# Kernel tuning notes

Hardware: AMD Instinct MI355X
Metric: run time of the kernel (lower is better)

## Reference

```python
import jax, jax.numpy as jnp
import numpy as np

N_NODES = 10000
N_EDGES = 320000
IN_DIM = 256
HIDDEN = 256
OUT_DIM = 128


def setup_inputs() -> dict:
    key = jax.random.key(0)
    k1, k2, k3, k4, k5, k6 = jax.random.split(key, 6)
    features = jax.random.normal(k1, (N_NODES, IN_DIM), dtype=jnp.float32)
    edge_src = jax.random.randint(k2, (N_EDGES,), 0, N_NODES, dtype=jnp.int64)
    edge_dst = jax.random.randint(k3, (N_EDGES,), 0, N_NODES, dtype=jnp.int64)
    edge_val = jax.random.uniform(k4, (N_EDGES,), dtype=jnp.float32)
    # Xavier-uniform weights as in nn.init.xavier_uniform_
    lim0 = float(np.sqrt(6.0 / (IN_DIM + HIDDEN)))
    lim1 = float(np.sqrt(6.0 / (HIDDEN + OUT_DIM)))
    W0 = jax.random.uniform(k5, (IN_DIM, HIDDEN), dtype=jnp.float32, minval=-lim0, maxval=lim0)
    W1 = jax.random.uniform(k6, (HIDDEN, OUT_DIM), dtype=jnp.float32, minval=-lim1, maxval=lim1)
    return {"features": features, "edge_src": edge_src, "edge_dst": edge_dst,
            "edge_val": edge_val, "W0": W0, "W1": W1}


def reference(features, edge_src, edge_dst, edge_val, W0, W1):
    # Sum over partition SpMMs in `broadcast` == full-graph SpMM: Z = A @ H
    n = features.shape[0]

    def spmm(h):
        msgs = edge_val[:, None] * h[edge_src]          # [E, d] gather + scale
        return jax.ops.segment_sum(msgs, edge_dst, num_segments=n)  # [N, d] scatter-add

    h = jax.nn.relu(spmm(features) @ W0)  # layer 0: SpMM -> GEMM -> ReLU
    out = spmm(h) @ W1                    # layer 1 (last): SpMM -> GEMM, no ReLU
    return out
```

## Files before the change

### kernel.cpp

```cpp
#include <hip/hip_runtime.h>

#define N_NODES 10000
#define IN_DIM 256
#define HIDDEN 256
#define OUT_DIM 128

typedef __attribute__((ext_vector_type(8))) short bf16x8;
typedef __attribute__((ext_vector_type(4))) float f32x4;
typedef __attribute__((ext_vector_type(4))) unsigned short u16x4;

__device__ __forceinline__ unsigned short f2bf(float x) {
  union { float f; unsigned u; } c; c.f = x;
  unsigned r = (c.u + 0x7FFFu + ((c.u >> 16) & 1u)) >> 16;
  return (unsigned short)r;
}
__device__ __forceinline__ float bf2f(unsigned short u) {
  union { unsigned u; float f; } c; c.u = ((unsigned)u) << 16;
  return c.f;
}

__global__ __launch_bounds__(256)
void hist_convW(const int* __restrict__ dst, int* __restrict__ cnt,
                const float* __restrict__ W0, const float* __restrict__ W1,
                unsigned short* __restrict__ W0t, unsigned short* __restrict__ W1t,
                int nE) {
  int gid = blockIdx.x * 256 + threadIdx.x;
  if (gid < nE) atomicAdd(&cnt[dst[gid]], 1);
  if (gid < IN_DIM * HIDDEN) {
    int k = gid & 255, n = gid >> 8;
    W0t[n * 256 + k] = f2bf(W0[k * 256 + n]);
  } else if (gid < IN_DIM * HIDDEN + HIDDEN * OUT_DIM) {
    int i = gid - IN_DIM * HIDDEN;
    int k = i & 255, n = i >> 8;
    W1t[n * 256 + k] = f2bf(W1[k * 128 + n]);
  }
}

__global__ __launch_bounds__(1024)
void scan_kernel(const int* __restrict__ cnt, int* __restrict__ rowptr,
                 int* __restrict__ rowcur) {
  const int t = threadIdx.x;
  const int lane = t & 63, wv = t >> 6;
  constexpr int PER = 10;
  const int base = t * PER;
  int c[PER];
  int sum = 0;
#pragma unroll
  for (int i = 0; i < PER; ++i) {
    int idx = base + i;
    c[i] = (idx < N_NODES) ? cnt[idx] : 0;
    sum += c[i];
  }
  int x = sum;
  for (int off = 1; off < 64; off <<= 1) {
    int y = __shfl_up(x, off);
    if (lane >= off) x += y;
  }
  __shared__ int wsum[16], wpre[16];
  if (lane == 63) wsum[wv] = x;
  __syncthreads();
  if (t == 0) {
    int run = 0;
#pragma unroll
    for (int i = 0; i < 16; ++i) { wpre[i] = run; run += wsum[i]; }
  }
  __syncthreads();
  int run = wpre[wv] + x - sum;
#pragma unroll
  for (int i = 0; i < PER; ++i) {
    int idx = base + i;
    if (idx < N_NODES) {
      rowptr[idx] = run;
      rowcur[idx] = run;
      run += c[i];
    }
  }
  if (t == 1023) rowptr[N_NODES] = run;
}

__global__ __launch_bounds__(256)
void bucket_kernel(const int* __restrict__ src, const int* __restrict__ dst,
                   const float* __restrict__ val, int* __restrict__ rowcur,
                   int2* __restrict__ edges, int nE) {
  int i = blockIdx.x * 256 + threadIdx.x;
  if (i < nE) {
    int d = dst[i];
    int p = atomicAdd(&rowcur[d], 1);
    edges[p] = make_int2(src[i], __float_as_int(val[i]));
  }
}

__global__ __launch_bounds__(256)
void gemm_mfma(const float* __restrict__ F, const unsigned short* __restrict__ Bt,
               unsigned short* __restrict__ C) {
  const int w = threadIdx.x >> 6;
  const int l = threadIdx.x & 63;
  const int r0 = blockIdx.y * 64 + w * 16;
  const int c0 = blockIdx.x * 64;
  const int arow = r0 + (l & 15);
  const int kof = (l >> 4) * 8;
  const bool rv = arow < N_NODES;
  const float* Ap = F + (size_t)arow * 256 + kof;
  f32x4 acc[4] = {};
#pragma unroll
  for (int k0 = 0; k0 < 256; k0 += 32) {
    bf16x8 af = {};
    if (rv) {
      float4 fa = *reinterpret_cast<const float4*>(Ap + k0);
      float4 fb = *reinterpret_cast<const float4*>(Ap + k0 + 4);
      af[0] = (short)f2bf(fa.x); af[1] = (short)f2bf(fa.y);
      af[2] = (short)f2bf(fa.z); af[3] = (short)f2bf(fa.w);
      af[4] = (short)f2bf(fb.x); af[5] = (short)f2bf(fb.y);
      af[6] = (short)f2bf(fb.z); af[7] = (short)f2bf(fb.w);
    }
#pragma unroll
    for (int j = 0; j < 4; ++j) {
      bf16x8 bfr = *reinterpret_cast<const bf16x8*>(
          Bt + (size_t)(c0 + j * 16 + (l & 15)) * 256 + k0 + kof);
      acc[j] = __builtin_amdgcn_mfma_f32_16x16x32_bf16(af, bfr, acc[j], 0, 0, 0);
    }
  }
  const int orow0 = r0 + ((l >> 4) << 2);
#pragma unroll
  for (int j = 0; j < 4; ++j) {
    const int col = c0 + j * 16 + (l & 15);
#pragma unroll
    for (int r = 0; r < 4; ++r) {
      int orow = orow0 + r;
      if (orow < N_NODES) C[(size_t)orow * HIDDEN + col] = f2bf(acc[j][r]);
    }
  }
}

__global__ __launch_bounds__(512)
void fused_spmm_gemm(const unsigned short* __restrict__ T0b,
                     const int2* __restrict__ edges,
                     const int* __restrict__ rp,
                     const unsigned short* __restrict__ W1t,
                     unsigned short* __restrict__ T1b) {
  __shared__ unsigned short Zs[16 * 256];
  const int wv = threadIdx.x >> 6;
  const int l  = threadIdx.x & 63;
  const int nb = blockIdx.x * 16;
  const unsigned short* Xl = T0b + l * 4;
#pragma unroll
  for (int i = 0; i < 2; ++i) {
    const int r = wv * 2 + i;
    const int node = nb + r;
    const int r0 = rp[node], r1 = rp[node + 1];
    float acc[4] = {};
    for (int base = r0; base < r1; base += 64) {
      int m = r1 - base; if (m > 64) m = 64;
      int2 me = make_int2(0, 0);
      if (base + l < r1) me = edges[base + l];
      int j = 0;
      for (; j + 4 <= m; j += 4) {
        int s0 = __shfl(me.x, j + 0), s1 = __shfl(me.x, j + 1);
        int s2 = __shfl(me.x, j + 2), s3 = __shfl(me.x, j + 3);
        float v0 = __int_as_float(__shfl(me.y, j + 0));
        float v1 = __int_as_float(__shfl(me.y, j + 1));
        float v2 = __int_as_float(__shfl(me.y, j + 2));
        float v3 = __int_as_float(__shfl(me.y, j + 3));
        u16x4 a = *reinterpret_cast<const u16x4*>(Xl + (size_t)s0 * 256);
        u16x4 b = *reinterpret_cast<const u16x4*>(Xl + (size_t)s1 * 256);
        u16x4 c = *reinterpret_cast<const u16x4*>(Xl + (size_t)s2 * 256);
        u16x4 d = *reinterpret_cast<const u16x4*>(Xl + (size_t)s3 * 256);
#pragma unroll
        for (int q = 0; q < 4; ++q) acc[q] = fmaf(v0, bf2f(a[q]), acc[q]);
#pragma unroll
        for (int q = 0; q < 4; ++q) acc[q] = fmaf(v1, bf2f(b[q]), acc[q]);
#pragma unroll
        for (int q = 0; q < 4; ++q) acc[q] = fmaf(v2, bf2f(c[q]), acc[q]);
#pragma unroll
        for (int q = 0; q < 4; ++q) acc[q] = fmaf(v3, bf2f(d[q]), acc[q]);
      }
      for (; j < m; ++j) {
        int s0 = __shfl(me.x, j);
        float v0 = __int_as_float(__shfl(me.y, j));
        u16x4 a = *reinterpret_cast<const u16x4*>(Xl + (size_t)s0 * 256);
#pragma unroll
        for (int q = 0; q < 4; ++q) acc[q] = fmaf(v0, bf2f(a[q]), acc[q]);
      }
    }
    u16x4 o;
#pragma unroll
    for (int q = 0; q < 4; ++q) o[q] = f2bf(fmaxf(acc[q], 0.f));
    int off = (r * 512 + l * 8) ^ ((r & 7) << 4);
    *reinterpret_cast<u16x4*>(reinterpret_cast<char*>(Zs) + off) = o;
  }
  __syncthreads();
  const int row = l & 15;
  const int kof = (l >> 4) * 8;
  const int cb = wv * 16;
  f32x4 acc2 = {};
#pragma unroll
  for (int k0 = 0; k0 < 256; k0 += 32) {
    int aoff = (row * 512 + (k0 + kof) * 2) ^ ((row & 7) << 4);
    bf16x8 af = *reinterpret_cast<const bf16x8*>(reinterpret_cast<const char*>(Zs) + aoff);
    bf16x8 bfr = *reinterpret_cast<const bf16x8*>(
        W1t + (size_t)(cb + row) * 256 + k0 + kof);
    acc2 = __builtin_amdgcn_mfma_f32_16x16x32_bf16(af, bfr, acc2, 0, 0, 0);
  }
  const int orow0 = (l >> 4) * 4;
  const int col = cb + row;
#pragma unroll
  for (int rr = 0; rr < 4; ++rr)
    T1b[(size_t)(nb + orow0 + rr) * OUT_DIM + col] = f2bf(acc2[rr]);
}

__global__ __launch_bounds__(256)
void spmm_out(const unsigned short* __restrict__ T1b,
              const int2* __restrict__ edges,
              const int* __restrict__ rp,
              float* __restrict__ out) {
  const int wv = threadIdx.x >> 6;
  const int lane = threadIdx.x & 63;
  const int half = lane >> 5;
  const int hl = lane & 31;
  const int node = blockIdx.x * 8 + wv * 2 + half;
  const int r0 = rp[node], r1 = rp[node + 1];
  float acc[4] = {};
  const unsigned short* Xl = T1b + hl * 4;
  for (int base = r0; base < r1; base += 32) {
    int m = r1 - base; if (m > 32) m = 32;
    int2 me = make_int2(0, 0);
    if (base + hl < r1) me = edges[base + hl];
    int j = 0;
    for (; j + 4 <= m; j += 4) {
      int s0 = __shfl(me.x, j + 0, 32), s1 = __shfl(me.x, j + 1, 32);
      int s2 = __shfl(me.x, j + 2, 32), s3 = __shfl(me.x, j + 3, 32);
      float v0 = __int_as_float(__shfl(me.y, j + 0, 32));
      float v1 = __int_as_float(__shfl(me.y, j + 1, 32));
      float v2 = __int_as_float(__shfl(me.y, j + 2, 32));
      float v3 = __int_as_float(__shfl(me.y, j + 3, 32));
      u16x4 a = *reinterpret_cast<const u16x4*>(Xl + (size_t)s0 * 128);
      u16x4 b = *reinterpret_cast<const u16x4*>(Xl + (size_t)s1 * 128);
      u16x4 c = *reinterpret_cast<const u16x4*>(Xl + (size_t)s2 * 128);
      u16x4 d = *reinterpret_cast<const u16x4*>(Xl + (size_t)s3 * 128);
#pragma unroll
      for (int q = 0; q < 4; ++q) acc[q] = fmaf(v0, bf2f(a[q]), acc[q]);
#pragma unroll
      for (int q = 0; q < 4; ++q) acc[q] = fmaf(v1, bf2f(b[q]), acc[q]);
#pragma unroll
      for (int q = 0; q < 4; ++q) acc[q] = fmaf(v2, bf2f(c[q]), acc[q]);
#pragma unroll
      for (int q = 0; q < 4; ++q) acc[q] = fmaf(v3, bf2f(d[q]), acc[q]);
    }
    for (; j < m; ++j) {
      int s0 = __shfl(me.x, j, 32);
      float v0 = __int_as_float(__shfl(me.y, j, 32));
      u16x4 a = *reinterpret_cast<const u16x4*>(Xl + (size_t)s0 * 128);
#pragma unroll
      for (int q = 0; q < 4; ++q) acc[q] = fmaf(v0, bf2f(a[q]), acc[q]);
    }
  }
  float4 o; o.x = acc[0]; o.y = acc[1]; o.z = acc[2]; o.w = acc[3];
  *reinterpret_cast<float4*>(out + (size_t)node * OUT_DIM + hl * 4) = o;
}

extern "C" void kernel_launch(void* const* d_in, const int* in_sizes, int n_in,
                              void* d_out, int out_size, void* d_ws, size_t ws_size,
                              hipStream_t stream) {
  const float* features = (const float*)d_in[0];
  const int*   esrc     = (const int*)d_in[1];
  const int*   edst     = (const int*)d_in[2];
  const float* evalv    = (const float*)d_in[3];
  const float* W0       = (const float*)d_in[4];
  const float* W1       = (const float*)d_in[5];
  const int nE = in_sizes[1];
  float* out = (float*)d_out;

  unsigned short* W0t = (unsigned short*)d_ws;
  unsigned short* W1t = W0t + (size_t)IN_DIM * HIDDEN;
  unsigned short* T0b = W1t + (size_t)OUT_DIM * HIDDEN;
  unsigned short* T1b = T0b + (size_t)N_NODES * HIDDEN;
  int2* edges  = (int2*)(T1b + (size_t)N_NODES * OUT_DIM);
  int* cnt     = (int*)(edges + nE);
  int* rowptr  = cnt + N_NODES;
  int* rowcur  = rowptr + N_NODES + 1;

  const int ebk = (nE + 255) / 256;

  hipMemsetAsync(cnt, 0, N_NODES * sizeof(int), stream);
  hist_convW<<<ebk, 256, 0, stream>>>(edst, cnt, W0, W1, W0t, W1t, nE);
  scan_kernel<<<1, 1024, 0, stream>>>(cnt, rowptr, rowcur);
  bucket_kernel<<<ebk, 256, 0, stream>>>(esrc, edst, evalv, rowcur, edges, nE);

  gemm_mfma<<<dim3(HIDDEN / 64, (N_NODES + 63) / 64), 256, 0, stream>>>(features, W0t, T0b);
  fused_spmm_gemm<<<N_NODES / 16, 512, 0, stream>>>(T0b, edges, rowptr, W1t, T1b);
  spmm_out<<<N_NODES / 8, 256, 0, stream>>>(T1b, edges, rowptr, out);
}
```

Baseline: 173.9 us.

## Merge all stages into one persistent cooperative kernel with grid syncs

Replaces the memset and six separate kernel launches with a single cooperative persistent kernel that walks through each stage and separates them with grid.sync(). The edge histogram now runs at the same time as the first dense GEMM, split across disjoint block groups. The fused SpMM+GEMM stage moves from 512-thread blocks to 256-thread blocks doing more work per wave. The goal is to remove launch gaps and tail idling between short kernels. In exchange it adds grid-wide barrier costs, caps occupancy through the cooperative launch size, and runs the row-pointer scan on a single block while the rest of the grid waits.

```diff
diff --git a/kernel.cpp b/kernel.cpp
--- a/kernel.cpp
+++ b/kernel.cpp
@@ -1,4 +1,7 @@
 #include <hip/hip_runtime.h>
+#include <hip/hip_cooperative_groups.h>
+
+namespace cg = cooperative_groups;
 
 #define N_NODES 10000
 #define IN_DIM 256
@@ -19,152 +22,223 @@
   return c.f;
 }
 
-__global__ __launch_bounds__(256)
-void hist_convW(const int* __restrict__ dst, int* __restrict__ cnt,
-                const float* __restrict__ W0, const float* __restrict__ W1,
-                unsigned short* __restrict__ W0t, unsigned short* __restrict__ W1t,
-                int nE) {
-  int gid = blockIdx.x * 256 + threadIdx.x;
-  if (gid < nE) atomicAdd(&cnt[dst[gid]], 1);
-  if (gid < IN_DIM * HIDDEN) {
-    int k = gid & 255, n = gid >> 8;
-    W0t[n * 256 + k] = f2bf(W0[k * 256 + n]);
-  } else if (gid < IN_DIM * HIDDEN + HIDDEN * OUT_DIM) {
-    int i = gid - IN_DIM * HIDDEN;
+__global__ __launch_bounds__(256, 3)
+void uber(const float* __restrict__ F, const int* __restrict__ esrc,
+          const int* __restrict__ edst, const float* __restrict__ evalv,
+          const float* __restrict__ W0, const float* __restrict__ W1,
+          float* __restrict__ out,
+          unsigned short* W0t, unsigned short* W1t,
+          unsigned short* T0b, unsigned short* T1b,
+          int2* edges, int* cnt, int* rowptr, int* rowcur, int nE) {
+  cg::grid_group grid = cg::this_grid();
+  __shared__ unsigned short Zs[16 * 256];
+  const int bid = blockIdx.x;
+  const int t = threadIdx.x;
+  const int gid0 = bid * 256 + t;
+  const int gstr = gridDim.x * 256;
+  const int wv = t >> 6;
+  const int l = t & 63;
+
+  for (int i = gid0; i < N_NODES; i += gstr) cnt[i] = 0;
+  for (int i = gid0; i < IN_DIM * HIDDEN; i += gstr) {
     int k = i & 255, n = i >> 8;
-    W1t[n * 256 + k] = f2bf(W1[k * 128 + n]);
-  }
-}
-
-__global__ __launch_bounds__(1024)
-void scan_kernel(const int* __restrict__ cnt, int* __restrict__ rowptr,
-                 int* __restrict__ rowcur) {
-  const int t = threadIdx.x;
-  const int lane = t & 63, wv = t >> 6;
-  constexpr int PER = 10;
-  const int base = t * PER;
-  int c[PER];
-  int sum = 0;
-#pragma unroll
-  for (int i = 0; i < PER; ++i) {
-    int idx = base + i;
-    c[i] = (idx < N_NODES) ? cnt[idx] : 0;
-    sum += c[i];
-  }
-  int x = sum;
-  for (int off = 1; off < 64; off <<= 1) {
-    int y = __shfl_up(x, off);
-    if (lane >= off) x += y;
-  }
-  __shared__ int wsum[16], wpre[16];
-  if (lane == 63) wsum[wv] = x;
-  __syncthreads();
-  if (t == 0) {
-    int run = 0;
-#pragma unroll
-    for (int i = 0; i < 16; ++i) { wpre[i] = run; run += wsum[i]; }
-  }
-  __syncthreads();
-  int run = wpre[wv] + x - sum;
-#pragma unroll
-  for (int i = 0; i < PER; ++i) {
-    int idx = base + i;
-    if (idx < N_NODES) {
-      rowptr[idx] = run;
-      rowcur[idx] = run;
-      run += c[i];
-    }
-  }
-  if (t == 1023) rowptr[N_NODES] = run;
-}
-
-__global__ __launch_bounds__(256)
-void bucket_kernel(const int* __restrict__ src, const int* __restrict__ dst,
-                   const float* __restrict__ val, int* __restrict__ rowcur,
-                   int2* __restrict__ edges, int nE) {
-  int i = blockIdx.x * 256 + threadIdx.x;
-  if (i < nE) {
-    int d = dst[i];
+    W0t[i] = f2bf(W0[k * 256 + n]);
+  }
+  for (int i = gid0; i < OUT_DIM * HIDDEN; i += gstr) {
+    int k = i & 255, n = i >> 8;
+    W1t[i] = f2bf(W1[k * 128 + n]);
+  }
+  grid.sync();
+
+  if (bid < 64) {
+    for (int i = gid0; i < nE; i += 64 * 256) atomicAdd(&cnt[edst[i]], 1);
+  } else {
+    for (int tile = bid - 64; tile < 628; tile += gridDim.x - 64) {
+      const int by = tile >> 2, bx = tile & 3;
+      const int r0t = by * 64 + wv * 16;
+      const int c0 = bx * 64;
+      const int arow = r0t + (l & 15);
+      const int kof = (l >> 4) * 8;
+      const bool rv = arow < N_NODES;
+      const float* Ap = F + (size_t)arow * 256 + kof;
+      f32x4 acc[4] = {};
+#pragma unroll
+      for (int k0 = 0; k0 < 256; k0 += 32) {
+        bf16x8 af = {};
+        if (rv) {
+          float4 fa = *reinterpret_cast<const float4*>(Ap + k0);
+          float4 fb = *reinterpret_cast<const float4*>(Ap + k0 + 4);
+          af[0] = (short)f2bf(fa.x); af[1] = (short)f2bf(fa.y);
+          af[2] = (short)f2bf(fa.z); af[3] = (short)f2bf(fa.w);
+          af[4] = (short)f2bf(fb.x); af[5] = (short)f2bf(fb.y);
+          af[6] = (short)f2bf(fb.z); af[7] = (short)f2bf(fb.w);
+        }
+#pragma unroll
+        for (int j = 0; j < 4; ++j) {
+          bf16x8 bfr = *reinterpret_cast<const bf16x8*>(
+              W0t + (size_t)(c0 + j * 16 + (l & 15)) * 256 + k0 + kof);
+          acc[j] = __builtin_amdgcn_mfma_f32_16x16x32_bf16(af, bfr, acc[j], 0, 0, 0);
+        }
+      }
+      const int orow0 = r0t + ((l >> 4) << 2);
+#pragma unroll
+      for (int j = 0; j < 4; ++j) {
+        const int col = c0 + j * 16 + (l & 15);
+#pragma unroll
+        for (int r = 0; r < 4; ++r) {
+          int orow = orow0 + r;
+          if (orow < N_NODES) T0b[(size_t)orow * HIDDEN + col] = f2bf(acc[j][r]);
+        }
+      }
+    }
+  }
+  grid.sync();
+
+  if (bid == 0) {
+    constexpr int PER = (N_NODES + 255) / 256;
+    const int base = t * PER;
+    int c[PER];
+    int sum = 0;
+#pragma unroll
+    for (int i = 0; i < PER; ++i) {
+      int idx = base + i;
+      c[i] = (idx < N_NODES) ? cnt[idx] : 0;
+      sum += c[i];
+    }
+    int x = sum;
+    for (int off = 1; off < 64; off <<= 1) {
+      int y = __shfl_up(x, off);
+      if (l >= off) x += y;
+    }
+    __shared__ int wsum[4], wpre[4];
+    if (l == 63) wsum[wv] = x;
+    __syncthreads();
+    if (t == 0) {
+      int run = 0;
+#pragma unroll
+      for (int i = 0; i < 4; ++i) { wpre[i] = run; run += wsum[i]; }
+    }
+    __syncthreads();
+    int run = wpre[wv] + x - sum;
+#pragma unroll
+    for (int i = 0; i < PER; ++i) {
+      int idx = base + i;
+      if (idx < N_NODES) {
+        rowptr[idx] = run;
+        rowcur[idx] = run;
+        run += c[i];
+      }
+    }
+    if (t == 255) rowptr[N_NODES] = run;
+  }
+  grid.sync();
+
+  for (int i = gid0; i < nE; i += gstr) {
+    int d = edst[i];
     int p = atomicAdd(&rowcur[d], 1);
-    edges[p] = make_int2(src[i], __float_as_int(val[i]));
-  }
-}
-
-__global__ __launch_bounds__(256)
-void gemm_mfma(const float* __restrict__ F, const unsigned short* __restrict__ Bt,
-               unsigned short* __restrict__ C) {
-  const int w = threadIdx.x >> 6;
-  const int l = threadIdx.x & 63;
-  const int r0 = blockIdx.y * 64 + w * 16;
-  const int c0 = blockIdx.x * 64;
-  const int arow = r0 + (l & 15);
-  const int kof = (l >> 4) * 8;
-  const bool rv = arow < N_NODES;
-  const float* Ap = F + (size_t)arow * 256 + kof;
-  f32x4 acc[4] = {};
-#pragma unroll
-  for (int k0 = 0; k0 < 256; k0 += 32) {
-    bf16x8 af = {};
-    if (rv) {
-      float4 fa = *reinterpret_cast<const float4*>(Ap + k0);
-      float4 fb = *reinterpret_cast<const float4*>(Ap + k0 + 4);
-      af[0] = (short)f2bf(fa.x); af[1] = (short)f2bf(fa.y);
-      af[2] = (short)f2bf(fa.z); af[3] = (short)f2bf(fa.w);
-      af[4] = (short)f2bf(fb.x); af[5] = (short)f2bf(fb.y);
-      af[6] = (short)f2bf(fb.z); af[7] = (short)f2bf(fb.w);
-    }
-#pragma unroll
-    for (int j = 0; j < 4; ++j) {
-      bf16x8 bfr = *reinterpret_cast<const bf16x8*>(
-          Bt + (size_t)(c0 + j * 16 + (l & 15)) * 256 + k0 + kof);
-      acc[j] = __builtin_amdgcn_mfma_f32_16x16x32_bf16(af, bfr, acc[j], 0, 0, 0);
-    }
-  }
-  const int orow0 = r0 + ((l >> 4) << 2);
-#pragma unroll
-  for (int j = 0; j < 4; ++j) {
-    const int col = c0 + j * 16 + (l & 15);
-#pragma unroll
-    for (int r = 0; r < 4; ++r) {
-      int orow = orow0 + r;
-      if (orow < N_NODES) C[(size_t)orow * HIDDEN + col] = f2bf(acc[j][r]);
-    }
-  }
-}
-
-__global__ __launch_bounds__(512)
-void fused_spmm_gemm(const unsigned short* __restrict__ T0b,
-                     const int2* __restrict__ edges,
-                     const int* __restrict__ rp,
-                     const unsigned short* __restrict__ W1t,
-                     unsigned short* __restrict__ T1b) {
-  __shared__ unsigned short Zs[16 * 256];
-  const int wv = threadIdx.x >> 6;
-  const int l  = threadIdx.x & 63;
-  const int nb = blockIdx.x * 16;
-  const unsigned short* Xl = T0b + l * 4;
-#pragma unroll
-  for (int i = 0; i < 2; ++i) {
-    const int r = wv * 2 + i;
-    const int node = nb + r;
-    const int r0 = rp[node], r1 = rp[node + 1];
+    edges[p] = make_int2(esrc[i], __float_as_int(evalv[i]));
+  }
+  grid.sync();
+
+  for (int tile = bid; tile < N_NODES / 16; tile += gridDim.x) {
+    const int nb = tile * 16;
+    const unsigned short* Xl = T0b + l * 4;
+#pragma unroll
+    for (int i = 0; i < 4; ++i) {
+      const int r = wv * 4 + i;
+      const int node = nb + r;
+      const int r0 = rowptr[node], r1 = rowptr[node + 1];
+      float acc[4] = {};
+      for (int base = r0; base < r1; base += 64) {
+        int m = r1 - base; if (m > 64) m = 64;
+        int2 me = make_int2(0, 0);
+        if (base + l < r1) me = edges[base + l];
+        int j = 0;
+        for (; j + 4 <= m; j += 4) {
+          int s0 = __shfl(me.x, j + 0), s1 = __shfl(me.x, j + 1);
+          int s2 = __shfl(me.x, j + 2), s3 = __shfl(me.x, j + 3);
+          float v0 = __int_as_float(__shfl(me.y, j + 0));
+          float v1 = __int_as_float(__shfl(me.y, j + 1));
+          float v2 = __int_as_float(__shfl(me.y, j + 2));
+          float v3 = __int_as_float(__shfl(me.y, j + 3));
+          u16x4 a = *reinterpret_cast<const u16x4*>(Xl + (size_t)s0 * 256);
+          u16x4 b = *reinterpret_cast<const u16x4*>(Xl + (size_t)s1 * 256);
+          u16x4 c = *reinterpret_cast<const u16x4*>(Xl + (size_t)s2 * 256);
+          u16x4 d = *reinterpret_cast<const u16x4*>(Xl + (size_t)s3 * 256);
+#pragma unroll
+          for (int q = 0; q < 4; ++q) acc[q] = fmaf(v0, bf2f(a[q]), acc[q]);
+#pragma unroll
+          for (int q = 0; q < 4; ++q) acc[q] = fmaf(v1, bf2f(b[q]), acc[q]);
+#pragma unroll
+          for (int q = 0; q < 4; ++q) acc[q] = fmaf(v2, bf2f(c[q]), acc[q]);
+#pragma unroll
+          for (int q = 0; q < 4; ++q) acc[q] = fmaf(v3, bf2f(d[q]), acc[q]);
+        }
+        for (; j < m; ++j) {
+          int s0 = __shfl(me.x, j);
+          float v0 = __int_as_float(__shfl(me.y, j));
+          u16x4 a = *reinterpret_cast<const u16x4*>(Xl + (size_t)s0 * 256);
+#pragma unroll
+          for (int q = 0; q < 4; ++q) acc[q] = fmaf(v0, bf2f(a[q]), acc[q]);
+        }
+      }
+      u16x4 o;
+#pragma unroll
+      for (int q = 0; q < 4; ++q) o[q] = f2bf(fmaxf(acc[q], 0.f));
+      int off = (r * 512 + l * 8) ^ ((r & 7) << 4);
+      *reinterpret_cast<u16x4*>(reinterpret_cast<char*>(Zs) + off) = o;
+    }
+    __syncthreads();
+    const int row = l & 15;
+    const int kof = (l >> 4) * 8;
+    const int cb = wv * 32;
+    f32x4 acc2[2] = {};
+#pragma unroll
+    for (int k0 = 0; k0 < 256; k0 += 32) {
+      int aoff = (row * 512 + (k0 + kof) * 2) ^ ((row & 7) << 4);
+      bf16x8 af = *reinterpret_cast<const bf16x8*>(reinterpret_cast<const char*>(Zs) + aoff);
+#pragma unroll
+      for (int j = 0; j < 2; ++j) {
+        bf16x8 bfr = *reinterpret_cast<const bf16x8*>(
+            W1t + (size_t)(cb + j * 16 + row) * 256 + k0 + kof);
+        acc2[j] = __builtin_amdgcn_mfma_f32_16x16x32_bf16(af, bfr, acc2[j], 0, 0, 0);
+      }
+    }
+    const int orow0 = (l >> 4) * 4;
+#pragma unroll
+    for (int j = 0; j < 2; ++j) {
+      const int col = cb + j * 16 + row;
+#pragma unroll
+      for (int rr = 0; rr < 4; ++rr)
+        T1b[(size_t)(nb + orow0 + rr) * OUT_DIM + col] = f2bf(acc2[j][rr]);
+    }
+    __syncthreads();
+  }
+  grid.sync();
+
+  for (int tile = bid; tile < N_NODES / 8; tile += gridDim.x) {
+    const int half = l >> 5;
+    const int hl = l & 31;
+    const int node = tile * 8 + wv * 2 + half;
+    const int r0 = rowptr[node], r1 = rowptr[node + 1];
     float acc[4] = {};
-    for (int base = r0; base < r1; base += 64) {
-      int m = r1 - base; if (m > 64) m = 64;
+    const unsigned short* Xl = T1b + hl * 4;
+    for (int base = r0; base < r1; base += 32) {
+      int m = r1 - base; if (m > 32) m = 32;
       int2 me = make_int2(0, 0);
-      if (base + l < r1) me = edges[base + l];
+      if (base + hl < r1) me = edges[base + hl];
       int j = 0;
       for (; j + 4 <= m; j += 4) {
-        int s0 = __shfl(me.x, j + 0), s1 = __shfl(me.x, j + 1);
-        int s2 = __shfl(me.x, j + 2), s3 = __shfl(me.x, j + 3);
-        float v0 = __int_as_float(__shfl(me.y, j + 0));
-        float v1 = __int_as_float(__shfl(me.y, j + 1));
-        float v2 = __int_as_float(__shfl(me.y, j + 2));
-        float v3 = __int_as_float(__shfl(me.y, j + 3));
-        u16x4 a = *reinterpret_cast<const u16x4*>(Xl + (size_t)s0 * 256);
-        u16x4 b = *reinterpret_cast<const u16x4*>(Xl + (size_t)s1 * 256);
-        u16x4 c = *reinterpret_cast<const u16x4*>(Xl + (size_t)s2 * 256);
-        u16x4 d = *reinterpret_cast<const u16x4*>(Xl + (size_t)s3 * 256);
+        int s0 = __shfl(me.x, j + 0, 32), s1 = __shfl(me.x, j + 1, 32);
+        int s2 = __shfl(me.x, j + 2, 32), s3 = __shfl(me.x, j + 3, 32);
+        float v0 = __int_as_float(__shfl(me.y, j + 0, 32));
+        float v1 = __int_as_float(__shfl(me.y, j + 1, 32));
+        float v2 = __int_as_float(__shfl(me.y, j + 2, 32));
+        float v3 = __int_as_float(__shfl(me.y, j + 3, 32));
+        u16x4 a = *reinterpret_cast<const u16x4*>(Xl + (size_t)s0 * 128);
+        u16x4 b = *reinterpret_cast<const u16x4*>(Xl + (size_t)s1 * 128);
+        u16x4 c = *reinterpret_cast<const u16x4*>(Xl + (size_t)s2 * 128);
+        u16x4 d = *reinterpret_cast<const u16x4*>(Xl + (size_t)s3 * 128);
 #pragma unroll
         for (int q = 0; q < 4; ++q) acc[q] = fmaf(v0, bf2f(a[q]), acc[q]);
 #pragma unroll
@@ -175,87 +249,16 @@
         for (int q = 0; q < 4; ++q) acc[q] = fmaf(v3, bf2f(d[q]), acc[q]);
       }
       for (; j < m; ++j) {
-        int s0 = __shfl(me.x, j);
-        float v0 = __int_as_float(__shfl(me.y, j));
-        u16x4 a = *reinterpret_cast<const u16x4*>(Xl + (size_t)s0 * 256);
+        int s0 = __shfl(me.x, j, 32);
+        float v0 = __int_as_float(__shfl(me.y, j, 32));
+        u16x4 a = *reinterpret_cast<const u16x4*>(Xl + (size_t)s0 * 128);
 #pragma unroll
         for (int q = 0; q < 4; ++q) acc[q] = fmaf(v0, bf2f(a[q]), acc[q]);
       }
     }
-    u16x4 o;
-#pragma unroll
-    for (int q = 0; q < 4; ++q) o[q] = f2bf(fmaxf(acc[q], 0.f));
-    int off = (r * 512 + l * 8) ^ ((r & 7) << 4);
-    *reinterpret_cast<u16x4*>(reinterpret_cast<char*>(Zs) + off) = o;
-  }
-  __syncthreads();
-  const int row = l & 15;
-  const int kof = (l >> 4) * 8;
-  const int cb = wv * 16;
-  f32x4 acc2 = {};
-#pragma unroll
-  for (int k0 = 0; k0 < 256; k0 += 32) {
-    int aoff = (row * 512 + (k0 + kof) * 2) ^ ((row & 7) << 4);
-    bf16x8 af = *reinterpret_cast<const bf16x8*>(reinterpret_cast<const char*>(Zs) + aoff);
-    bf16x8 bfr = *reinterpret_cast<const bf16x8*>(
-        W1t + (size_t)(cb + row) * 256 + k0 + kof);
-    acc2 = __builtin_amdgcn_mfma_f32_16x16x32_bf16(af, bfr, acc2, 0, 0, 0);
-  }
-  const int orow0 = (l >> 4) * 4;
-  const int col = cb + row;
-#pragma unroll
-  for (int rr = 0; rr < 4; ++rr)
-    T1b[(size_t)(nb + orow0 + rr) * OUT_DIM + col] = f2bf(acc2[rr]);
-}
-
-__global__ __launch_bounds__(256)
-void spmm_out(const unsigned short* __restrict__ T1b,
-              const int2* __restrict__ edges,
-              const int* __restrict__ rp,
-              float* __restrict__ out) {
-  const int wv = threadIdx.x >> 6;
-  const int lane = threadIdx.x & 63;
-  const int half = lane >> 5;
-  const int hl = lane & 31;
-  const int node = blockIdx.x * 8 + wv * 2 + half;
-  const int r0 = rp[node], r1 = rp[node + 1];
-  float acc[4] = {};
-  const unsigned short* Xl = T1b + hl * 4;
-  for (int base = r0; base < r1; base += 32) {
-    int m = r1 - base; if (m > 32) m = 32;
-    int2 me = make_int2(0, 0);
-    if (base + hl < r1) me = edges[base + hl];
-    int j = 0;
-    for (; j + 4 <= m; j += 4) {
-      int s0 = __shfl(me.x, j + 0, 32), s1 = __shfl(me.x, j + 1, 32);
-      int s2 = __shfl(me.x, j + 2, 32), s3 = __shfl(me.x, j + 3, 32);
-      float v0 = __int_as_float(__shfl(me.y, j + 0, 32));
-      float v1 = __int_as_float(__shfl(me.y, j + 1, 32));
-      float v2 = __int_as_float(__shfl(me.y, j + 2, 32));
-      float v3 = __int_as_float(__shfl(me.y, j + 3, 32));
-      u16x4 a = *reinterpret_cast<const u16x4*>(Xl + (size_t)s0 * 128);
-      u16x4 b = *reinterpret_cast<const u16x4*>(Xl + (size_t)s1 * 128);
-      u16x4 c = *reinterpret_cast<const u16x4*>(Xl + (size_t)s2 * 128);
-      u16x4 d = *reinterpret_cast<const u16x4*>(Xl + (size_t)s3 * 128);
-#pragma unroll
-      for (int q = 0; q < 4; ++q) acc[q] = fmaf(v0, bf2f(a[q]), acc[q]);
-#pragma unroll
-      for (int q = 0; q < 4; ++q) acc[q] = fmaf(v1, bf2f(b[q]), acc[q]);
-#pragma unroll
-      for (int q = 0; q < 4; ++q) acc[q] = fmaf(v2, bf2f(c[q]), acc[q]);
-#pragma unroll
-      for (int q = 0; q < 4; ++q) acc[q] = fmaf(v3, bf2f(d[q]), acc[q]);
-    }
-    for (; j < m; ++j) {
-      int s0 = __shfl(me.x, j, 32);
-      float v0 = __int_as_float(__shfl(me.y, j, 32));
-      u16x4 a = *reinterpret_cast<const u16x4*>(Xl + (size_t)s0 * 128);
-#pragma unroll
-      for (int q = 0; q < 4; ++q) acc[q] = fmaf(v0, bf2f(a[q]), acc[q]);
-    }
-  }
-  float4 o; o.x = acc[0]; o.y = acc[1]; o.z = acc[2]; o.w = acc[3];
-  *reinterpret_cast<float4*>(out + (size_t)node * OUT_DIM + hl * 4) = o;
+    float4 o; o.x = acc[0]; o.y = acc[1]; o.z = acc[2]; o.w = acc[3];
+    *reinterpret_cast<float4*>(out + (size_t)node * OUT_DIM + hl * 4) = o;
+  }
 }
 
 extern "C" void kernel_launch(void* const* d_in, const int* in_sizes, int n_in,
@@ -267,7 +270,7 @@
   const float* evalv    = (const float*)d_in[3];
   const float* W0       = (const float*)d_in[4];
   const float* W1       = (const float*)d_in[5];
-  const int nE = in_sizes[1];
+  int nE = in_sizes[1];
   float* out = (float*)d_out;
 
   unsigned short* W0t = (unsigned short*)d_ws;
@@ -279,14 +282,18 @@
   int* rowptr  = cnt + N_NODES;
   int* rowcur  = rowptr + N_NODES + 1;
 
-  const int ebk = (nE + 255) / 256;
-
-  hipMemsetAsync(cnt, 0, N_NODES * sizeof(int), stream);
-  hist_convW<<<ebk, 256, 0, stream>>>(edst, cnt, W0, W1, W0t, W1t, nE);
-  scan_kernel<<<1, 1024, 0, stream>>>(cnt, rowptr, rowcur);
-  bucket_kernel<<<ebk, 256, 0, stream>>>(esrc, edst, evalv, rowcur, edges, nE);
-
-  gemm_mfma<<<dim3(HIDDEN / 64, (N_NODES + 63) / 64), 256, 0, stream>>>(features, W0t, T0b);
-  fused_spmm_gemm<<<N_NODES / 16, 512, 0, stream>>>(T0b, edges, rowptr, W1t, T1b);
-  spmm_out<<<N_NODES / 8, 256, 0, stream>>>(T1b, edges, rowptr, out);
-}
+  int perCU = 0;
+  hipError_t e = hipOccupancyMaxActiveBlocksPerMultiprocessor(
+      &perCU, reinterpret_cast<const void*>(uber), 256, 0);
+  int blocks = (e == hipSuccess && perCU > 0) ? perCU * 256 : 512;
+  if (blocks > 768) blocks = 768;
+
+  void* args[] = {
+    (void*)&features, (void*)&esrc, (void*)&edst, (void*)&evalv,
+    (void*)&W0, (void*)&W1, (void*)&out,
+    (void*)&W0t, (void*)&W1t, (void*)&T0b, (void*)&T1b,
+    (void*)&edges, (void*)&cnt, (void*)&rowptr, (void*)&rowcur, (void*)&nE
+  };
+  hipLaunchCooperativeKernel(reinterpret_cast<const void*>(uber),
+                             dim3(blocks), dim3(256), args, 0, stream);
+}
```

After: 502.2 us. +188.8%, slower.
